# Kernel tuning notes

Measured on AMD Instinct MI355X. Metric: run time of the kernel, lower is better.

Reference implementation:

```python
import jax, jax.numpy as jnp
import numpy as np

BATCH, D, H = 8192, 512, 2048
DT = 0.1
N_STEPS = 10  # t0=0.0 -> t1=1.0 with dt0=0.1, ConstantStepSize


def setup_inputs() -> dict:
    key = jax.random.key(0)
    k0, k1, k2 = jax.random.split(key, 3)
    y0 = jax.random.normal(k0, (BATCH, D), dtype=jnp.float32)
    # fan-in scaled init to keep the tanh MLP vector field well-conditioned
    W1 = jax.random.normal(k1, (D, H), dtype=jnp.float32) / np.sqrt(D).astype(np.float32)
    b1 = jnp.zeros((H,), dtype=jnp.float32)
    W2 = jax.random.normal(k2, (H, D), dtype=jnp.float32) / np.sqrt(H).astype(np.float32)
    b2 = jnp.zeros((D,), dtype=jnp.float32)
    return {"y0": y0, "W1": W1, "b1": b1, "W2": W2, "b2": b2}


def reference(y0, W1, b1, W2, b2):
    dt = jnp.float32(DT)

    def f(t, y):  # autonomous MLP vector field; t unused but kept for ODE form
        return jnp.tanh(y @ W1 + b1) @ W2 + b2

    def heun_step(y, t):
        k1 = f(t, y)
        k2 = f(t + dt, y + dt * k1)
        return y + (0.5 * dt) * (k1 + k2), None

    ts = jnp.arange(N_STEPS, dtype=jnp.float32) * dt
    y1, _ = jax.lax.scan(heun_step, y0, ts)
    return y1  # solution.ys[0] at t1=1.0
```

## Files before the change

### kernel.cpp

```cpp
#include <hip/hip_runtime.h>
#include <hip/hip_bf16.h>
#include <cstdint>


#define BATCHN 8192
#define DDIM 512
#define HDIM 2048
#define CW 512
#define NCH (HDIM / CW)

typedef short short8 __attribute__((ext_vector_type(8)));
typedef float floatx16 __attribute__((ext_vector_type(16)));
typedef int int4v __attribute__((ext_vector_type(4)));
typedef int intx16 __attribute__((ext_vector_type(16)));

__device__ __forceinline__ unsigned short f2bf(float f) {
  union { __hip_bfloat16 h; unsigned short u; } cv;
  cv.h = __float2bfloat16(f);
  return cv.u;
}

__device__ __forceinline__ float fast_tanh(float x) {
  float e = __expf(2.0f * x);
  return 1.0f - 2.0f / (e + 1.0f);
}


__global__ __launch_bounds__(1024, 4) void fused_feval(
    const unsigned short* __restrict__ yPack,
    const unsigned short* __restrict__ w1p,
    const signed char* __restrict__ w2p8,
    const float* __restrict__ qsArr,
    const float* __restrict__ b1,
    const float* __restrict__ b2,
    const float* __restrict__ stateIn,
    float* __restrict__ stateOut,
    unsigned short* __restrict__ outPack,
    int epi) {
  __shared__ unsigned short yA[32 * 512];
  __shared__ signed char hA8[2][32 * CW];

  const int tid  = threadIdx.x;
  const int lane = tid & 63;
  const int w    = tid >> 6;
  const int c31  = lane & 31;
  const int lhi  = lane >> 5;
  const int blk  = blockIdx.x;
  const int B0   = blk * 32;

  {
    const unsigned short* src = yPack + (size_t)blk * (32 * 512);
    __builtin_amdgcn_global_load_lds(
        (const __attribute__((address_space(1))) void*)(uintptr_t)(src + (size_t)tid * 8),
        (__attribute__((address_space(3))) void*)(uint32_t)(uintptr_t)&yA[tid * 8],
        16, 0, 0);
    __builtin_amdgcn_global_load_lds(
        (const __attribute__((address_space(1))) void*)(uintptr_t)(src + (size_t)(1024 + tid) * 8),
        (__attribute__((address_space(3))) void*)(uint32_t)(uintptr_t)&yA[(1024 + tid) * 8],
        16, 0, 0);
  }

  float bb1v[NCH];
#pragma unroll
  for (int c = 0; c < NCH; ++c) bb1v[c] = b1[c * CW + w * 32 + c31];

  __syncthreads();

  intx16 accY = {};

#pragma unroll
  for (int c = 0; c < NCH; ++c) {
    floatx16 acc1 = {};
    const unsigned short* w1b =
        w1p + ((size_t)((c * 16 + w) * 32) * 64 + lane) * 8;
#pragma unroll
    for (int ks = 0; ks < 32; ++ks) {
      short8 a = *(const short8*)&yA[(ks * 64 + lane) * 8];
      short8 b = *(const short8*)(w1b + (size_t)ks * 512);
      acc1 = __builtin_amdgcn_mfma_f32_32x32x16_bf16(a, b, acc1, 0, 0, 0);
    }

    {
      signed char* hbuf = hA8[c & 1];
      const float bb = bb1v[c];
      const int khalf = (c31 >> 4) << 5;
      const int jj8 = c31 & 15;
      const int mhi = lhi * 4;
#pragma unroll
      for (int reg = 0; reg < 16; ++reg) {
        const int m = (reg & 3) + 8 * (reg >> 2) + mhi;
        const float hv = fast_tanh(acc1[reg] + bb);
        hbuf[(w * 64 + khalf + m) * 16 + jj8] =
            (signed char)(int)rintf(hv * 127.0f);
      }
    }

    if (c > 0) {
      const int cc = c - 1;
      const signed char* hp = hA8[cc & 1];
      const signed char* w2b =
          w2p8 + ((size_t)(w * 64 + cc * 16) * 64 + lane) * 16;
#pragma unroll
      for (int ks = 0; ks < 16; ++ks) {
        int4v a = *(const int4v*)&hp[(ks * 64 + lane) * 16];
        int4v b = *(const int4v*)(w2b + (size_t)ks * 1024);
        accY = __builtin_amdgcn_mfma_i32_32x32x32_i8(a, b, accY, 0, 0, 0);
      }
    }
    __syncthreads();
  }
  {
    const int cc = NCH - 1;
    const signed char* hp = hA8[cc & 1];
    const signed char* w2b =
        w2p8 + ((size_t)(w * 64 + cc * 16) * 64 + lane) * 16;
#pragma unroll
    for (int ks = 0; ks < 16; ++ks) {
      int4v a = *(const int4v*)&hp[(ks * 64 + lane) * 16];
      int4v b = *(const int4v*)(w2b + (size_t)ks * 1024);
      accY = __builtin_amdgcn_mfma_i32_32x32x32_i8(a, b, accY, 0, 0, 0);
    }
  }
  __syncthreads();

  {
    unsigned short* pbuf = (unsigned short*)&hA8[0][0];
    const int ncol = w * 32 + c31;
    const float sc = qsArr[ncol] * (1.0f / 127.0f);
    const float bb = b2[ncol];
    const int ksf = ncol >> 4;
    const int lh  = (ncol >> 3) & 1;
    const int jj  = ncol & 7;
    const int mhi = lhi * 4;
#pragma unroll
    for (int reg = 0; reg < 16; ++reg) {
      const int mrow = (reg & 3) + 8 * (reg >> 2) + mhi;
      const int row = B0 + mrow;
      const size_t idx = (size_t)row * DDIM + ncol;
      const float v = (float)accY[reg] * sc + bb;
      float nv;
      if (epi == 1) {
        const float y = stateIn[idx];
        stateOut[idx] = y + 0.05f * v;
        nv = y + 0.1f * v;
      } else {
        const float yn = stateIn[idx] + 0.05f * v;
        stateOut[idx] = yn;
        nv = yn;
      }
      pbuf[(ksf * 64 + (mrow + 32 * lh)) * 8 + jj] = f2bf(nv);
    }
    __syncthreads();
    unsigned short* dst = outPack + (size_t)blk * (32 * 512);
#pragma unroll
    for (int p = 0; p < 2; ++p) {
      short8 v = *(const short8*)&pbuf[(size_t)(p * 1024 + tid) * 8];
      *(short8*)&dst[(size_t)(p * 1024 + tid) * 8] = v;
    }
  }
}

__global__ void pack_b(const float* __restrict__ src, unsigned short* __restrict__ dst,
                       int KB, int N) {
  const int t = blockIdx.x * 256 + threadIdx.x;
  const int lane = t & 63, f = t >> 6;
  const int nb = f / KB, kb = f % KB;
  const int k0 = kb * 16 + (lane >> 5) * 8, n = nb * 32 + (lane & 31);
  short8 v;
#pragma unroll
  for (int j = 0; j < 8; ++j)
    v[j] = (short)f2bf(src[(size_t)(k0 + j) * N + n]);
  *(short8*)&dst[(size_t)t * 8] = v;
}

__global__ void zero_cm(unsigned* __restrict__ cm) { cm[threadIdx.x] = 0u; }

__global__ void colmax_w2(const float* __restrict__ w2, unsigned* __restrict__ cm) {
  const int n = threadIdx.x;
  const int k0 = blockIdx.x * 16;
  float m = 0.0f;
#pragma unroll
  for (int i = 0; i < 16; ++i) m = fmaxf(m, fabsf(w2[(size_t)(k0 + i) * DDIM + n]));
  atomicMax(&cm[n], __float_as_uint(m));
}

__global__ void pack_w2i8(const float* __restrict__ w2, const unsigned* __restrict__ cm,
                          signed char* __restrict__ dst, float* __restrict__ qsArr) {
  const int t = blockIdx.x * 256 + threadIdx.x;
  const int lane = t & 63, f = t >> 6;
  const int nb = f >> 6, kb = f & 63;
  const int n = nb * 32 + (lane & 31);
  const int k0 = kb * 32 + (lane >> 5) * 16;
  float qs = __uint_as_float(cm[n]) * (1.0f / 127.0f);
  if (qs <= 0.0f) qs = 1.0f;
  if (kb == 0 && (lane >> 5) == 0) qsArr[n] = qs;
  const float inv = 1.0f / qs;
  union { signed char b[16]; int4v v; } o;
#pragma unroll
  for (int j = 0; j < 16; ++j)
    o.b[j] = (signed char)(int)rintf(w2[(size_t)(k0 + j) * DDIM + n] * inv);
  *(int4v*)&dst[(size_t)t * 16] = o.v;
}

__global__ void pack_y(const float* __restrict__ y0, float* __restrict__ yF,
                       unsigned short* __restrict__ ypk) {
  const int t = blockIdx.x * 256 + threadIdx.x;
  const int lane = t & 63, f = t >> 6;
  const int rb = f >> 5, ks = f & 31;
  const int row = rb * 32 + (lane & 31), c0 = ks * 16 + (lane >> 5) * 8;
  short8 v;
#pragma unroll
  for (int j = 0; j < 8; ++j) {
    const float x = y0[(size_t)row * DDIM + c0 + j];
    yF[(size_t)row * DDIM + c0 + j] = x;
    v[j] = (short)f2bf(x);
  }
  *(short8*)&ypk[(size_t)t * 8] = v;
}

extern "C" void kernel_launch(void* const* d_in, const int* in_sizes, int n_in,
                              void* d_out, int out_size, void* d_ws, size_t ws_size,
                              hipStream_t stream) {
  const float* y0 = (const float*)d_in[0];
  const float* W1 = (const float*)d_in[1];
  const float* b1 = (const float*)d_in[2];
  const float* W2 = (const float*)d_in[3];
  const float* b2 = (const float*)d_in[4];

  char* ws = (char*)d_ws;
  float*          yF   = (float*)(ws);
  float*          pF   = (float*)(ws + (size_t)(16u << 20));
  unsigned short* ypk  = (unsigned short*)(ws + (size_t)(32u << 20));
  unsigned short* ympk = (unsigned short*)(ws + (size_t)(40u << 20));
  unsigned short* w1p  = (unsigned short*)(ws + (size_t)(48u << 20));
  signed char*    w2p8 = (signed char*)(ws + (size_t)(50u << 20));
  float*          qsArr = (float*)(ws + (size_t)(51u << 20));
  unsigned*       cmU   = (unsigned*)(ws + (size_t)(51u << 20) + 4096);

  zero_cm<<<1, 512, 0, stream>>>(cmU);
  colmax_w2<<<128, 512, 0, stream>>>(W2, cmU);
  pack_b<<<512, 256, 0, stream>>>(W1, w1p, 32, HDIM);
  pack_w2i8<<<256, 256, 0, stream>>>(W2, cmU, w2p8, qsArr);
  pack_y<<<2048, 256, 0, stream>>>(y0, yF, ypk);

  const dim3 grid(256), blkd(1024);
  for (int s = 0; s < 10; ++s) {
    fused_feval<<<grid, blkd, 0, stream>>>(ypk, w1p, w2p8, qsArr, b1, b2, yF, pF, ympk, 1);
    float* yOut = (s == 9) ? (float*)d_out : yF;
    fused_feval<<<grid, blkd, 0, stream>>>(ympk, w1p, w2p8, qsArr, b1, b2, pF, yOut, ypk, 2);
  }
}
```

Baseline: 988.9 us.

## Quantize first GEMM to int8 with per-row activation and per-column weight scales

Switches the y@W1 GEMM from bf16 MFMA to int8 MFMA. W1 is quantized per column, and the state is quantized per row, with the row maxima found inside the kernel epilogue through shuffles and LDS atomics. This halves the K-steps and the byte traffic of the first GEMM and halves the packed state size. The cost is more quantization error in the ODE integration, plus extra reduction work and a sync in the epilogue.

```diff
diff --git a/kernel.cpp b/kernel.cpp
--- a/kernel.cpp
+++ b/kernel.cpp
@@ -10,15 +10,8 @@
 #define NCH (HDIM / CW)
 
 typedef short short8 __attribute__((ext_vector_type(8)));
-typedef float floatx16 __attribute__((ext_vector_type(16)));
 typedef int int4v __attribute__((ext_vector_type(4)));
 typedef int intx16 __attribute__((ext_vector_type(16)));
-
-__device__ __forceinline__ unsigned short f2bf(float f) {
-  union { __hip_bfloat16 h; unsigned short u; } cv;
-  cv.h = __float2bfloat16(f);
-  return cv.u;
-}
 
 __device__ __forceinline__ float fast_tanh(float x) {
   float e = __expf(2.0f * x);
@@ -27,18 +20,22 @@
 
 
 __global__ __launch_bounds__(1024, 4) void fused_feval(
-    const unsigned short* __restrict__ yPack,
-    const unsigned short* __restrict__ w1p,
+    const signed char* __restrict__ in8,
+    const float* __restrict__ rsIn,
+    const signed char* __restrict__ w1p8,
+    const float* __restrict__ csW1,
     const signed char* __restrict__ w2p8,
-    const float* __restrict__ qsArr,
+    const float* __restrict__ qs2,
     const float* __restrict__ b1,
     const float* __restrict__ b2,
     const float* __restrict__ stateIn,
     float* __restrict__ stateOut,
-    unsigned short* __restrict__ outPack,
+    signed char* __restrict__ out8,
+    float* __restrict__ rsOut,
     int epi) {
-  __shared__ unsigned short yA[32 * 512];
+  __shared__ signed char yA8[32 * 512];
   __shared__ signed char hA8[2][32 * CW];
+  __shared__ unsigned rowmaxU[32];
 
   const int tid  = threadIdx.x;
   const int lane = tid & 63;
@@ -49,20 +46,29 @@
   const int B0   = blk * 32;
 
   {
-    const unsigned short* src = yPack + (size_t)blk * (32 * 512);
+    const signed char* src = in8 + (size_t)blk * 16384;
     __builtin_amdgcn_global_load_lds(
-        (const __attribute__((address_space(1))) void*)(uintptr_t)(src + (size_t)tid * 8),
-        (__attribute__((address_space(3))) void*)(uint32_t)(uintptr_t)&yA[tid * 8],
+        (const __attribute__((address_space(1))) void*)(uintptr_t)(src + (size_t)tid * 16),
+        (__attribute__((address_space(3))) void*)(uint32_t)(uintptr_t)&yA8[tid * 16],
         16, 0, 0);
-    __builtin_amdgcn_global_load_lds(
-        (const __attribute__((address_space(1))) void*)(uintptr_t)(src + (size_t)(1024 + tid) * 8),
-        (__attribute__((address_space(3))) void*)(uint32_t)(uintptr_t)&yA[(1024 + tid) * 8],
-        16, 0, 0);
-  }
-
-  float bb1v[NCH];
-#pragma unroll
-  for (int c = 0; c < NCH; ++c) bb1v[c] = b1[c * CW + w * 32 + c31];
+  }
+  if (tid < 32) rowmaxU[tid] = 0u;
+
+  const int ncol = w * 32 + c31;
+  float bb1v[NCH], cw1v[NCH];
+#pragma unroll
+  for (int c = 0; c < NCH; ++c) {
+    bb1v[c] = b1[c * CW + ncol];
+    cw1v[c] = csW1[c * CW + ncol];
+  }
+  const float bb2 = b2[ncol];
+  const float sc2 = qs2[ncol] * (1.0f / 127.0f);
+  float rs_in[16];
+#pragma unroll
+  for (int reg = 0; reg < 16; ++reg) {
+    const int mrow = (reg & 3) + 8 * (reg >> 2) + lhi * 4;
+    rs_in[reg] = rsIn[B0 + mrow];
+  }
 
   __syncthreads();
 
@@ -70,26 +76,28 @@
 
 #pragma unroll
   for (int c = 0; c < NCH; ++c) {
-    floatx16 acc1 = {};
-    const unsigned short* w1b =
-        w1p + ((size_t)((c * 16 + w) * 32) * 64 + lane) * 8;
-#pragma unroll
-    for (int ks = 0; ks < 32; ++ks) {
-      short8 a = *(const short8*)&yA[(ks * 64 + lane) * 8];
-      short8 b = *(const short8*)(w1b + (size_t)ks * 512);
-      acc1 = __builtin_amdgcn_mfma_f32_32x32x16_bf16(a, b, acc1, 0, 0, 0);
+    intx16 acc1 = {};
+    const signed char* w1b =
+        w1p8 + ((size_t)((c * 16 + w) * 16) * 64 + lane) * 16;
+#pragma unroll
+    for (int ks = 0; ks < 16; ++ks) {
+      int4v a = *(const int4v*)&yA8[(ks * 64 + lane) * 16];
+      int4v b = *(const int4v*)(w1b + (size_t)ks * 1024);
+      acc1 = __builtin_amdgcn_mfma_i32_32x32x32_i8(a, b, acc1, 0, 0, 0);
     }
 
     {
       signed char* hbuf = hA8[c & 1];
       const float bb = bb1v[c];
+      const float fa = cw1v[c];
       const int khalf = (c31 >> 4) << 5;
       const int jj8 = c31 & 15;
       const int mhi = lhi * 4;
 #pragma unroll
       for (int reg = 0; reg < 16; ++reg) {
         const int m = (reg & 3) + 8 * (reg >> 2) + mhi;
-        const float hv = fast_tanh(acc1[reg] + bb);
+        const float z = (float)acc1[reg] * (rs_in[reg] * fa) + bb;
+        const float hv = fast_tanh(z);
         hbuf[(w * 64 + khalf + m) * 16 + jj8] =
             (signed char)(int)rintf(hv * 127.0f);
       }
@@ -121,101 +129,124 @@
       accY = __builtin_amdgcn_mfma_i32_32x32x32_i8(a, b, accY, 0, 0, 0);
     }
   }
-  __syncthreads();
-
-  {
-    unsigned short* pbuf = (unsigned short*)&hA8[0][0];
-    const int ncol = w * 32 + c31;
-    const float sc = qsArr[ncol] * (1.0f / 127.0f);
-    const float bb = b2[ncol];
-    const int ksf = ncol >> 4;
-    const int lh  = (ncol >> 3) & 1;
-    const int jj  = ncol & 7;
+
+  float nv[16];
+  {
     const int mhi = lhi * 4;
 #pragma unroll
     for (int reg = 0; reg < 16; ++reg) {
       const int mrow = (reg & 3) + 8 * (reg >> 2) + mhi;
-      const int row = B0 + mrow;
-      const size_t idx = (size_t)row * DDIM + ncol;
-      const float v = (float)accY[reg] * sc + bb;
-      float nv;
+      const size_t idx = (size_t)(B0 + mrow) * DDIM + ncol;
+      const float v = (float)accY[reg] * sc2 + bb2;
       if (epi == 1) {
         const float y = stateIn[idx];
         stateOut[idx] = y + 0.05f * v;
-        nv = y + 0.1f * v;
+        nv[reg] = y + 0.1f * v;
       } else {
         const float yn = stateIn[idx] + 0.05f * v;
         stateOut[idx] = yn;
-        nv = yn;
+        nv[reg] = yn;
       }
-      pbuf[(ksf * 64 + (mrow + 32 * lh)) * 8 + jj] = f2bf(nv);
+      float am = fabsf(nv[reg]);
+      am = fmaxf(am, __shfl_xor(am, 1));
+      am = fmaxf(am, __shfl_xor(am, 2));
+      am = fmaxf(am, __shfl_xor(am, 4));
+      am = fmaxf(am, __shfl_xor(am, 8));
+      am = fmaxf(am, __shfl_xor(am, 16));
+      if (c31 == 0) atomicMax(&rowmaxU[mrow], __float_as_uint(am));
+    }
+  }
+  __syncthreads();
+
+  {
+    signed char* pbuf8 = &hA8[0][0];
+    const int khalf = (c31 >> 4) << 5;
+    const int jj8 = c31 & 15;
+    const int mhi = lhi * 4;
+#pragma unroll
+    for (int reg = 0; reg < 16; ++reg) {
+      const int mrow = (reg & 3) + 8 * (reg >> 2) + mhi;
+      const float mx = __uint_as_float(rowmaxU[mrow]);
+      const float inv = (mx > 0.0f) ? (127.0f / mx) : 0.0f;
+      pbuf8[(w * 64 + khalf + mrow) * 16 + jj8] =
+          (signed char)(int)rintf(nv[reg] * inv);
+    }
+    if (tid < 32) {
+      const float mx = __uint_as_float(rowmaxU[tid]);
+      rsOut[B0 + tid] = ((mx > 0.0f) ? mx : 127.0f) * (1.0f / 127.0f);
     }
     __syncthreads();
-    unsigned short* dst = outPack + (size_t)blk * (32 * 512);
-#pragma unroll
-    for (int p = 0; p < 2; ++p) {
-      short8 v = *(const short8*)&pbuf[(size_t)(p * 1024 + tid) * 8];
-      *(short8*)&dst[(size_t)(p * 1024 + tid) * 8] = v;
-    }
-  }
-}
-
-__global__ void pack_b(const float* __restrict__ src, unsigned short* __restrict__ dst,
-                       int KB, int N) {
+    signed char* dst = out8 + (size_t)blk * 16384;
+    *(int4v*)&dst[(size_t)tid * 16] = *(const int4v*)&pbuf8[(size_t)tid * 16];
+  }
+}
+
+
+__global__ void zero_u(unsigned* __restrict__ p, int n) {
+  const int i = blockIdx.x * 1024 + threadIdx.x;
+  if (i < n) p[i] = 0u;
+}
+
+__global__ void colmax_g(const float* __restrict__ src, unsigned* __restrict__ cm,
+                         int N) {
+  const int n = blockIdx.y * blockDim.x + threadIdx.x;
+  const int k0 = blockIdx.x * 16;
+  float m = 0.0f;
+#pragma unroll
+  for (int i = 0; i < 16; ++i) m = fmaxf(m, fabsf(src[(size_t)(k0 + i) * N + n]));
+  atomicMax(&cm[n], __float_as_uint(m));
+}
+
+__global__ void pack_bi8(const float* __restrict__ src, const unsigned* __restrict__ cm,
+                         signed char* __restrict__ dst, float* __restrict__ scArr,
+                         int KB, int N) {
   const int t = blockIdx.x * 256 + threadIdx.x;
   const int lane = t & 63, f = t >> 6;
   const int nb = f / KB, kb = f % KB;
-  const int k0 = kb * 16 + (lane >> 5) * 8, n = nb * 32 + (lane & 31);
-  short8 v;
-#pragma unroll
-  for (int j = 0; j < 8; ++j)
-    v[j] = (short)f2bf(src[(size_t)(k0 + j) * N + n]);
-  *(short8*)&dst[(size_t)t * 8] = v;
-}
-
-__global__ void zero_cm(unsigned* __restrict__ cm) { cm[threadIdx.x] = 0u; }
-
-__global__ void colmax_w2(const float* __restrict__ w2, unsigned* __restrict__ cm) {
-  const int n = threadIdx.x;
-  const int k0 = blockIdx.x * 16;
-  float m = 0.0f;
-#pragma unroll
-  for (int i = 0; i < 16; ++i) m = fmaxf(m, fabsf(w2[(size_t)(k0 + i) * DDIM + n]));
-  atomicMax(&cm[n], __float_as_uint(m));
-}
-
-__global__ void pack_w2i8(const float* __restrict__ w2, const unsigned* __restrict__ cm,
-                          signed char* __restrict__ dst, float* __restrict__ qsArr) {
-  const int t = blockIdx.x * 256 + threadIdx.x;
-  const int lane = t & 63, f = t >> 6;
-  const int nb = f >> 6, kb = f & 63;
   const int n = nb * 32 + (lane & 31);
   const int k0 = kb * 32 + (lane >> 5) * 16;
-  float qs = __uint_as_float(cm[n]) * (1.0f / 127.0f);
-  if (qs <= 0.0f) qs = 1.0f;
-  if (kb == 0 && (lane >> 5) == 0) qsArr[n] = qs;
+  const float mx = __uint_as_float(cm[n]);
+  const float qs = (mx > 0.0f) ? mx * (1.0f / 127.0f) : 1.0f;
+  if (kb == 0 && (lane >> 5) == 0) scArr[n] = qs;
   const float inv = 1.0f / qs;
   union { signed char b[16]; int4v v; } o;
 #pragma unroll
   for (int j = 0; j < 16; ++j)
-    o.b[j] = (signed char)(int)rintf(w2[(size_t)(k0 + j) * DDIM + n] * inv);
+    o.b[j] = (signed char)(int)rintf(src[(size_t)(k0 + j) * N + n] * inv);
   *(int4v*)&dst[(size_t)t * 16] = o.v;
 }
 
-__global__ void pack_y(const float* __restrict__ y0, float* __restrict__ yF,
-                       unsigned short* __restrict__ ypk) {
+__global__ void rowmax_y(const float* __restrict__ y0, float* __restrict__ rs) {
+  const int tid = threadIdx.x;
+  const int row = blockIdx.x * 32 + (tid >> 4);
+  const int c0 = (tid & 15) * 32;
+  float m = 0.0f;
+#pragma unroll
+  for (int j = 0; j < 32; ++j)
+    m = fmaxf(m, fabsf(y0[(size_t)row * DDIM + c0 + j]));
+  m = fmaxf(m, __shfl_xor(m, 1));
+  m = fmaxf(m, __shfl_xor(m, 2));
+  m = fmaxf(m, __shfl_xor(m, 4));
+  m = fmaxf(m, __shfl_xor(m, 8));
+  if ((tid & 15) == 0) rs[row] = ((m > 0.0f) ? m : 127.0f) * (1.0f / 127.0f);
+}
+
+__global__ void pack_y8(const float* __restrict__ y0, const float* __restrict__ rs,
+                        float* __restrict__ yF, signed char* __restrict__ dst) {
   const int t = blockIdx.x * 256 + threadIdx.x;
-  const int lane = t & 63, f = t >> 6;
-  const int rb = f >> 5, ks = f & 31;
-  const int row = rb * 32 + (lane & 31), c0 = ks * 16 + (lane >> 5) * 8;
-  short8 v;
-#pragma unroll
-  for (int j = 0; j < 8; ++j) {
+  const int u = t & 1023, slab = t >> 10;
+  const int f = u >> 6, lane = u & 63;
+  const int row = slab * 32 + (lane & 31);
+  const int c0 = f * 32 + (lane >> 5) * 16;
+  const float inv = 1.0f / rs[row];
+  union { signed char b[16]; int4v v; } o;
+#pragma unroll
+  for (int j = 0; j < 16; ++j) {
     const float x = y0[(size_t)row * DDIM + c0 + j];
     yF[(size_t)row * DDIM + c0 + j] = x;
-    v[j] = (short)f2bf(x);
-  }
-  *(short8*)&ypk[(size_t)t * 8] = v;
+    o.b[j] = (signed char)(int)rintf(x * inv);
+  }
+  *(int4v*)&dst[(size_t)t * 16] = o.v;
 }
 
 extern "C" void kernel_launch(void* const* d_in, const int* in_sizes, int n_in,
@@ -228,25 +259,32 @@
   const float* b2 = (const float*)d_in[4];
 
   char* ws = (char*)d_ws;
-  float*          yF   = (float*)(ws);
-  float*          pF   = (float*)(ws + (size_t)(16u << 20));
-  unsigned short* ypk  = (unsigned short*)(ws + (size_t)(32u << 20));
-  unsigned short* ympk = (unsigned short*)(ws + (size_t)(40u << 20));
-  unsigned short* w1p  = (unsigned short*)(ws + (size_t)(48u << 20));
-  signed char*    w2p8 = (signed char*)(ws + (size_t)(50u << 20));
-  float*          qsArr = (float*)(ws + (size_t)(51u << 20));
-  unsigned*       cmU   = (unsigned*)(ws + (size_t)(51u << 20) + 4096);
-
-  zero_cm<<<1, 512, 0, stream>>>(cmU);
-  colmax_w2<<<128, 512, 0, stream>>>(W2, cmU);
-  pack_b<<<512, 256, 0, stream>>>(W1, w1p, 32, HDIM);
-  pack_w2i8<<<256, 256, 0, stream>>>(W2, cmU, w2p8, qsArr);
-  pack_y<<<2048, 256, 0, stream>>>(y0, yF, ypk);
+  float*       yF    = (float*)(ws);
+  float*       pF    = (float*)(ws + (size_t)(16u << 20));
+  signed char* ypk8  = (signed char*)(ws + (size_t)(32u << 20));
+  signed char* ympk8 = (signed char*)(ws + (size_t)(36u << 20));
+  signed char* w1p8  = (signed char*)(ws + (size_t)(40u << 20));
+  signed char* w2p8  = (signed char*)(ws + (size_t)(41u << 20));
+  float*       csW1  = (float*)(ws + (size_t)(42u << 20));
+  float*       qs2   = (float*)(ws + (size_t)(42u << 20) + 16384);
+  unsigned*    cmU   = (unsigned*)(ws + (size_t)(42u << 20) + 32768);
+  float*       rsA   = (float*)(ws + (size_t)(43u << 20));
+  float*       rsB   = (float*)(ws + (size_t)(43u << 20) + 65536);
+
+  zero_u<<<3, 1024, 0, stream>>>(cmU, 2560);
+  colmax_g<<<dim3(32, 4), 512, 0, stream>>>(W1, cmU, HDIM);
+  colmax_g<<<dim3(128, 1), 512, 0, stream>>>(W2, cmU + 2048, DDIM);
+  pack_bi8<<<256, 256, 0, stream>>>(W1, cmU, w1p8, csW1, 16, HDIM);
+  pack_bi8<<<256, 256, 0, stream>>>(W2, cmU + 2048, w2p8, qs2, 64, DDIM);
+  rowmax_y<<<256, 512, 0, stream>>>(y0, rsA);
+  pack_y8<<<1024, 256, 0, stream>>>(y0, rsA, yF, ypk8);
 
   const dim3 grid(256), blkd(1024);
   for (int s = 0; s < 10; ++s) {
-    fused_feval<<<grid, blkd, 0, stream>>>(ypk, w1p, w2p8, qsArr, b1, b2, yF, pF, ympk, 1);
+    fused_feval<<<grid, blkd, 0, stream>>>(ypk8, rsA, w1p8, csW1, w2p8, qs2,
+                                           b1, b2, yF, pF, ympk8, rsB, 1);
     float* yOut = (s == 9) ? (float*)d_out : yF;
-    fused_feval<<<grid, blkd, 0, stream>>>(ympk, w1p, w2p8, qsArr, b1, b2, pF, yOut, ypk, 2);
-  }
-}
+    fused_feval<<<grid, blkd, 0, stream>>>(ympk8, rsB, w1p8, csW1, w2p8, qs2,
+                                           b1, b2, pF, yOut, ypk8, rsA, 2);
+  }
+}
```

Result: faster. 931.3 us (-5.8%).
